# Optimization experiments

Hardware: AMD Instinct MI355X
Metric: run time of the kernel (lower is better)

Reference implementation:

```python
import jax, jax.numpy as jnp
import numpy as np

N_USER = 25000
N_ITEM = 25000
N = N_USER + N_ITEM
E = 1_250_000
D = 64
L = 3
B = 4096


def setup_inputs() -> dict:
    key = jax.random.key(0)
    ks = jax.random.split(key, 11)
    emb = jax.random.normal(ks[0], (N, D), dtype=jnp.float32) * 0.1
    w1_w = jax.random.normal(ks[1], (L, D, D), dtype=jnp.float32) / np.sqrt(D)
    w1_b = jax.random.normal(ks[2], (L, D), dtype=jnp.float32) * 0.01
    w2_w = jax.random.normal(ks[3], (L, D, D), dtype=jnp.float32) / np.sqrt(D)
    w2_b = jax.random.normal(ks[4], (L, D), dtype=jnp.float32) * 0.01
    # normalized-laplacian-like nonneg values
    vals = jax.random.uniform(ks[5], (E,), dtype=jnp.float32) * 0.1
    rows = jax.random.randint(ks[6], (E,), 0, N, dtype=jnp.int32)
    cols = jax.random.randint(ks[7], (E,), 0, N, dtype=jnp.int32)
    user = jax.random.randint(ks[8], (B,), 0, N_USER, dtype=jnp.int32)
    pos = jax.random.randint(ks[9], (B,), 0, N, dtype=jnp.int32)
    neg = jax.random.randint(ks[10], (B,), 0, N, dtype=jnp.int32)
    return {"emb": emb, "w1_w": w1_w, "w1_b": w1_b, "w2_w": w2_w,
            "w2_b": w2_b, "vals": vals, "rows": rows, "cols": cols,
            "user": user, "pos": pos, "neg": neg}


def _spmm(vals, rows, cols, x):
    # sparse [N,N] @ dense [N,D] via gather + segment_sum
    msg = vals[:, None] * x[cols]          # [E, D]
    return jax.ops.segment_sum(msg, rows, num_segments=N)  # [N, D]


def reference(emb, w1_w, w1_b, w2_w, w2_b, vals, rows, cols, user, pos, neg):
    user_embs = [emb[user]]
    pos_embs = [emb[pos]]
    neg_embs = [emb[neg]]
    for l in range(L):
        agg = _spmm(vals, rows, cols, emb)                # sp.mm(laplacian, emb)
        # (laplacian + identity) @ emb == agg + emb
        sx = (agg + emb) @ w1_w[l].T + w1_b[l]
        ox = agg * (emb @ w2_w[l].T + w2_b[l])
        emb = jax.nn.leaky_relu(sx + ox, negative_slope=0.01)
        user_embs.append(emb[user])
        pos_embs.append(emb[pos])
        neg_embs.append(emb[neg])
    user_e = jnp.concatenate(user_embs, axis=-1)          # [B, (L+1)*D]
    pos_e = jnp.concatenate(pos_embs, axis=-1)
    neg_e = jnp.concatenate(neg_embs, axis=-1)
    pos_logits = jnp.einsum('id,id->i', user_e, pos_e)
    neg_logits = jnp.einsum('id,id->i', user_e, neg_e)
    # -log(sigmoid(diff)).sum(), computed stably
    return -jnp.sum(jax.nn.log_sigmoid(pos_logits - neg_logits))
```

## Files before the change

kernel.cpp:

```cpp
#include <hip/hip_runtime.h>
#include <hip/hip_fp16.h>
#include <math.h>

#define N_NODES 50000
#define EDGES   1250000
#define DIM     64
#define NLAYER  3
#define BATCH   4096
#define NSLOTS  (3 * BATCH)

#define NBUCK 196
#define RPB   256
#define NABLK 512
#define BCAP  7424

typedef unsigned int uint32;
typedef _Float16 f16x8 __attribute__((ext_vector_type(8)));
typedef float f32x4 __attribute__((ext_vector_type(4)));

static __device__ __forceinline__ ushort f2h(float f) {
    return __half_as_ushort(__float2half(f));
}
static __device__ __forceinline__ float h2f(ushort u) {
    return __half2float(__ushort_as_half(u));
}

static __device__ __forceinline__ int slot_node(int slot,
                                                const int* __restrict__ user,
                                                const int* __restrict__ pos,
                                                const int* __restrict__ neg) {
    if (slot < BATCH) return user[slot];
    if (slot < 2 * BATCH) return pos[slot - BATCH];
    return neg[slot - 2 * BATCH];
}


#define HP_F2H   512
#define HP_DOTS  3637
#define HP_TOTAL 4661

__global__ __launch_bounds__(256) void histprep_kernel(const int* __restrict__ rows,
                                                       int* __restrict__ bhist,
                                                       const float* __restrict__ emb,
                                                       ushort* __restrict__ xh,
                                                       const int* __restrict__ user,
                                                       const int* __restrict__ pos,
                                                       const int* __restrict__ neg,
                                                       float* __restrict__ dots,
                                                       float* __restrict__ out) {
    __shared__ int h[NBUCK];
    int blk = blockIdx.x;
    int tid = threadIdx.x;
    if (blk < HP_F2H) {
        if (blk == 0 && tid == 0) out[0] = 0.f;
        for (int i = tid; i < NBUCK; i += 256) h[i] = 0;
        __syncthreads();
        int per = (EDGES + NABLK - 1) / NABLK;
        int e0 = blk * per;
        int e1 = min(e0 + per, EDGES);
        for (int e = e0 + tid; e < e1; e += 256)
            atomicAdd(&h[rows[e] >> 8], 1);
        __syncthreads();
        for (int i = tid; i < NBUCK; i += 256)
            bhist[(size_t)i * NABLK + blk] = h[i];
    } else if (blk < HP_DOTS) {
        int i = (blk - HP_F2H) * 256 + tid;
        float4 v = ((const float4*)emb)[i];
        ushort4 hh;
        hh.x = f2h(v.x); hh.y = f2h(v.y); hh.z = f2h(v.z); hh.w = f2h(v.w);
        ((ushort4*)xh)[i] = hh;
    } else {
        int lane = tid & 63;
        int i = (blk - HP_DOTS) * 4 + (tid >> 6);
        int ui = user[i], pi = pos[i], ni = neg[i];
        float u = emb[(size_t)ui * DIM + lane];
        float p = emb[(size_t)pi * DIM + lane];
        float n = emb[(size_t)ni * DIM + lane];
        float v = u * (p - n);
#pragma unroll
        for (int off = 32; off; off >>= 1) v += __shfl_xor(v, off);
        if (lane == 0) dots[i] = v;
    }
}


__global__ __launch_bounds__(512) void boffs_kernel(const int* __restrict__ bhist,
                                                    int* __restrict__ boffs) {
    __shared__ int sbase[256];
    __shared__ int wred[8];
    int b = blockIdx.x;
    int tid = threadIdx.x;
    int lane = tid & 63, wid = tid >> 6;

    int tot = 0;
    if (tid < NBUCK) {
        const int* p = bhist + (size_t)tid * NABLK;
        for (int k = 0; k < NABLK; ++k) tot += p[k];
    }
    int sB = tot;
    if (tid < 256) {
#pragma unroll
        for (int off = 1; off < 64; off <<= 1) {
            int tt = __shfl_up(sB, off);
            if (lane >= off) sB += tt;
        }
        if (lane == 63) wred[wid] = sB;
    }
    __syncthreads();
    if (tid == 0) {
        int a = 0;
#pragma unroll
        for (int i = 0; i < 4; ++i) { int tt = wred[i]; wred[i] = a; a += tt; }
    }
    __syncthreads();
    if (tid < 256) sbase[tid] = wred[wid] + sB - tot;
    __syncthreads();
    int base = sbase[b];
    __syncthreads();

    int v = bhist[(size_t)b * NABLK + tid];
    int s = v;
#pragma unroll
    for (int off = 1; off < 64; off <<= 1) {
        int tt = __shfl_up(s, off);
        if (lane >= off) s += tt;
    }
    if (lane == 63) wred[wid] = s;
    __syncthreads();
    if (tid == 0) {
        int a = 0;
#pragma unroll
        for (int i = 0; i < 8; ++i) { int tt = wred[i]; wred[i] = a; a += tt; }
    }
    __syncthreads();
    boffs[(size_t)b * NABLK + tid] = base + wred[wid] + s - v;
}


__global__ __launch_bounds__(256) void bucket_scatter_kernel(const int* __restrict__ rows,
                                                             const int* __restrict__ cols,
                                                             const float* __restrict__ vals,
                                                             const int* __restrict__ boffs,
                                                             int2* __restrict__ staging) {
    __shared__ int cur[NBUCK];
    for (int t = threadIdx.x; t < NBUCK; t += 256)
        cur[t] = boffs[(size_t)t * NABLK + blockIdx.x];
    __syncthreads();
    int per = (EDGES + NABLK - 1) / NABLK;
    int e0 = blockIdx.x * per;
    int e1 = min(e0 + per, EDGES);
    for (int e = e0 + threadIdx.x; e < e1; e += 256) {
        int r = rows[e];
        int p = atomicAdd(&cur[r >> 8], 1);
        staging[p] = make_int2(((r & 255) << 16) | cols[e], __float_as_int(vals[e]));
    }
}


__global__ __launch_bounds__(512) void csr_build_kernel(const int* __restrict__ boffs,
                                                        const int2* __restrict__ staging,
                                                        int* __restrict__ row_ptr,
                                                        uint32* __restrict__ csr) {
    __shared__ int2 sedge[BCAP];
    __shared__ int rcur[RPB];
    __shared__ int wred[4];
    int b = blockIdx.x;
    int base = boffs[(size_t)b * NABLK];
    int end = (b == NBUCK - 1) ? EDGES : boffs[(size_t)(b + 1) * NABLK];
    int cnt = end - base;
    bool inlds = (cnt <= BCAP);
    int tid = threadIdx.x;
    int lane = tid & 63, wid = tid >> 6;
    if (tid < RPB) rcur[tid] = 0;
    __syncthreads();
    if (inlds) {
        for (int p = tid; p < cnt; p += 512) {
            int2 e = staging[base + p];
            sedge[p] = e;
            atomicAdd(&rcur[e.x >> 16], 1);
        }
    } else {
        for (int p = base + tid; p < end; p += 512)
            atomicAdd(&rcur[staging[p].x >> 16], 1);
    }
    __syncthreads();
    int v = 0, s = 0;
    if (tid < RPB) {
        v = rcur[tid];
        s = v;
#pragma unroll
        for (int off = 1; off < 64; off <<= 1) {
            int t = __shfl_up(s, off);
            if (lane >= off) s += t;
        }
        if (lane == 63) wred[wid] = s;
    }
    __syncthreads();
    if (tid == 0) {
        int a = 0;
#pragma unroll
        for (int i = 0; i < 4; ++i) { int t = wred[i]; wred[i] = a; a += t; }
    }
    __syncthreads();
    if (tid < RPB) {
        int excl = wred[wid] + s - v;
        rcur[tid] = base + excl;
        int row = b * RPB + tid;
        if (row < N_NODES) row_ptr[row] = base + excl;
    }
    if (b == NBUCK - 1 && tid == 0) row_ptr[N_NODES] = EDGES;
    __syncthreads();
    if (inlds) {
        for (int p = tid; p < cnt; p += 512) {
            int2 e = sedge[p];
            int pos = atomicAdd(&rcur[e.x >> 16], 1);
            csr[pos] = ((uint32)(e.x & 0xFFFF) << 16) | (uint32)f2h(__int_as_float(e.y));
        }
    } else {
        for (int p = base + tid; p < end; p += 512) {
            int2 e = staging[p];
            int pos = atomicAdd(&rcur[e.x >> 16], 1);
            csr[pos] = ((uint32)(e.x & 0xFFFF) << 16) | (uint32)f2h(__int_as_float(e.y));
        }
    }
}


static __device__ __forceinline__ void spmm_row(const uint32* __restrict__ csr,
                                                const ushort* __restrict__ xh,
                                                int p0, int p1, int g, int sl,
                                                float* a) {
#define SPMM_ACC(E, X)                                                     \
    {                                                                      \
        float vv = h2f((ushort)((E) & 0xFFFF));                            \
        a[0] += vv * h2f((ushort)((X).x & 0xFFFF));                        \
        a[1] += vv * h2f((ushort)((X).x >> 16));                           \
        a[2] += vv * h2f((ushort)((X).y & 0xFFFF));                        \
        a[3] += vv * h2f((ushort)((X).y >> 16));                           \
        a[4] += vv * h2f((ushort)((X).z & 0xFFFF));                        \
        a[5] += vv * h2f((ushort)((X).z >> 16));                           \
        a[6] += vv * h2f((ushort)((X).w & 0xFFFF));                        \
        a[7] += vv * h2f((ushort)((X).w >> 16));                           \
    }
    int p = p0;
    for (; p + 32 <= p1; p += 32) {
        uint32 e0 = csr[p + g];
        uint32 e1 = csr[p + 8 + g];
        uint32 e2 = csr[p + 16 + g];
        uint32 e3 = csr[p + 24 + g];
        uint4 x0 = *(const uint4*)(xh + (size_t)(e0 >> 16) * DIM + sl * 8);
        uint4 x1 = *(const uint4*)(xh + (size_t)(e1 >> 16) * DIM + sl * 8);
        uint4 x2 = *(const uint4*)(xh + (size_t)(e2 >> 16) * DIM + sl * 8);
        uint4 x3 = *(const uint4*)(xh + (size_t)(e3 >> 16) * DIM + sl * 8);
        SPMM_ACC(e0, x0);
        SPMM_ACC(e1, x1);
        SPMM_ACC(e2, x2);
        SPMM_ACC(e3, x3);
    }
    for (; p + 8 <= p1; p += 8) {
        uint32 ea = csr[p + g];
        uint4 xa = *(const uint4*)(xh + (size_t)(ea >> 16) * DIM + sl * 8);
        SPMM_ACC(ea, xa);
    }
    if (p + g < p1) {
        uint32 ea = csr[p + g];
        uint4 xa = *(const uint4*)(xh + (size_t)(ea >> 16) * DIM + sl * 8);
        SPMM_ACC(ea, xa);
    }
#undef SPMM_ACC
#pragma unroll
    for (int m = 8; m <= 32; m <<= 1) {
        a[0] += __shfl_xor(a[0], m); a[1] += __shfl_xor(a[1], m);
        a[2] += __shfl_xor(a[2], m); a[3] += __shfl_xor(a[3], m);
        a[4] += __shfl_xor(a[4], m); a[5] += __shfl_xor(a[5], m);
        a[6] += __shfl_xor(a[6], m); a[7] += __shfl_xor(a[7], m);
    }
}

static __device__ __forceinline__ void spmm_store(ushort* dst, const float* a, int lane) {
    if (lane < 8) {
        ushort t[8];
        t[0] = f2h(a[0]); t[1] = f2h(a[1]); t[2] = f2h(a[2]); t[3] = f2h(a[3]);
        t[4] = f2h(a[4]); t[5] = f2h(a[5]); t[6] = f2h(a[6]); t[7] = f2h(a[7]);
        *(uint4*)(dst + lane * 8) = *(uint4*)t;
    }
}

static __device__ __forceinline__ void dots_tail(const ushort* __restrict__ xh,
                                                 const int* __restrict__ user,
                                                 const int* __restrict__ pos,
                                                 const int* __restrict__ neg,
                                                 float* __restrict__ dots,
                                                 int i, int lane) {
    int ui = user[i], pi = pos[i], ni = neg[i];
    float u = h2f(xh[(size_t)ui * DIM + lane]);
    float p = h2f(xh[(size_t)pi * DIM + lane]);
    float n = h2f(xh[(size_t)ni * DIM + lane]);
    float v = u * (p - n);
#pragma unroll
    for (int off = 32; off; off >>= 1) v += __shfl_xor(v, off);
    if (lane == 0) dots[i] = v;
}


__global__ __launch_bounds__(256) void spmm_kernel(const int* __restrict__ row_ptr,
                                                   const uint32* __restrict__ csr,
                                                   const ushort* __restrict__ xh,
                                                   ushort* __restrict__ aggh,
                                                   const int* __restrict__ user,
                                                   const int* __restrict__ pos,
                                                   const int* __restrict__ neg,
                                                   float* __restrict__ dots,
                                                   int nsb) {
    int lane = threadIdx.x & 63;
    if ((int)blockIdx.x >= nsb) {
        int i = (blockIdx.x - nsb) * 4 + (threadIdx.x >> 6);
        dots_tail(xh, user, pos, neg, dots, i, lane);
        return;
    }
    int row = blockIdx.x * 4 + (threadIdx.x >> 6);
    int p0 = row_ptr[row], p1 = row_ptr[row + 1];
    float a[8] = {};
    spmm_row(csr, xh, p0, p1, lane >> 3, lane & 7, a);
    spmm_store(aggh + (size_t)row * DIM, a, lane);
}


__global__ __launch_bounds__(256) void spmm_slots_kernel(const int* __restrict__ row_ptr,
                                                         const uint32* __restrict__ csr,
                                                         const ushort* __restrict__ xh,
                                                         ushort* __restrict__ aggh_slot,
                                                         const int* __restrict__ user,
                                                         const int* __restrict__ pos,
                                                         const int* __restrict__ neg,
                                                         float* __restrict__ dots,
                                                         int nsb) {
    int lane = threadIdx.x & 63;
    if ((int)blockIdx.x >= nsb) {
        int i = (blockIdx.x - nsb) * 4 + (threadIdx.x >> 6);
        dots_tail(xh, user, pos, neg, dots, i, lane);
        return;
    }
    int slot = blockIdx.x * 4 + (threadIdx.x >> 6);
    int node = slot_node(slot, user, pos, neg);
    int p0 = row_ptr[node], p1 = row_ptr[node + 1];
    float a[8] = {};
    spmm_row(csr, xh, p0, p1, lane >> 3, lane & 7, a);
    spmm_store(aggh_slot + (size_t)slot * DIM, a, lane);
}


template <int IS_SLOT>
static __device__ __forceinline__ void dense_body(const ushort* __restrict__ xh_in,
                                                  const ushort* __restrict__ aggh,
                                                  const float* __restrict__ w1,
                                                  const float* __restrict__ w2,
                                                  const float* __restrict__ b1,
                                                  const float* __restrict__ b2,
                                                  ushort* __restrict__ yh,
                                                  const int* __restrict__ user,
                                                  const int* __restrict__ pos,
                                                  const int* __restrict__ neg) {
    __shared__ ushort xs[64 * 64];
    __shared__ ushort xc[64 * 64];
    __shared__ ushort w1s[64 * 64];
    __shared__ ushort w2s[64 * 64];

    int tid = threadIdx.x;
    int n0 = blockIdx.x * 64;

    {
        int rr = tid >> 2;
        int jq = (tid & 3) << 4;
        int sw = rr & 7;
        int b0 = jq >> 3;
        int o0 = rr * 64 + (((b0 + 0) ^ sw) << 3);
        int o1 = rr * 64 + (((b0 + 1) ^ sw) << 3);

        {
            const float* w1r = w1 + rr * 64 + jq;
            const float* w2r = w2 + rr * 64 + jq;
            ushort t1[16], t2[16];
#pragma unroll
            for (int k = 0; k < 4; ++k) {
                float4 a = ((const float4*)w1r)[k];
                float4 b = ((const float4*)w2r)[k];
                t1[k * 4 + 0] = f2h(a.x); t1[k * 4 + 1] = f2h(a.y);
                t1[k * 4 + 2] = f2h(a.z); t1[k * 4 + 3] = f2h(a.w);
                t2[k * 4 + 0] = f2h(b.x); t2[k * 4 + 1] = f2h(b.y);
                t2[k * 4 + 2] = f2h(b.z); t2[k * 4 + 3] = f2h(b.w);
            }
            *(uint4*)&w1s[o0] = *(uint4*)&t1[0];
            *(uint4*)&w1s[o1] = *(uint4*)&t1[8];
            *(uint4*)&w2s[o0] = *(uint4*)&t2[0];
            *(uint4*)&w2s[o1] = *(uint4*)&t2[8];
        }
        {
            int rowid = n0 + rr;
            int xnode, arow;
            if (IS_SLOT) {
                xnode = slot_node(rowid, user, pos, neg);
                arow = rowid;
            } else {
                xnode = (rowid < N_NODES) ? rowid : (N_NODES - 1);
                arow = xnode;
            }
            const ushort* ar = aggh + (size_t)arow * DIM + jq;
            const ushort* xr = xh_in + (size_t)xnode * DIM + jq;
            ushort txs[16], txc[16];
#pragma unroll
            for (int k = 0; k < 2; ++k) {
                uint4 xv = ((const uint4*)xr)[k];
                uint4 av = ((const uint4*)ar)[k];
                uint32 xw[4] = {xv.x, xv.y, xv.z, xv.w};
                uint32 aw[4] = {av.x, av.y, av.z, av.w};
#pragma unroll
                for (int q = 0; q < 4; ++q) {
                    ushort xlo = (ushort)(xw[q] & 0xFFFF);
                    ushort xhi = (ushort)(xw[q] >> 16);
                    ushort alo = (ushort)(aw[q] & 0xFFFF);
                    ushort ahi = (ushort)(aw[q] >> 16);
                    int e = k * 8 + q * 2;
                    txc[e] = xlo; txc[e + 1] = xhi;
                    txs[e] = f2h(h2f(xlo) + h2f(alo));
                    txs[e + 1] = f2h(h2f(xhi) + h2f(ahi));
                }
            }
            *(uint4*)&xs[o0] = *(uint4*)&txs[0];
            *(uint4*)&xs[o1] = *(uint4*)&txs[8];
            *(uint4*)&xc[o0] = *(uint4*)&txc[0];
            *(uint4*)&xc[o1] = *(uint4*)&txc[8];
        }
    }
    __syncthreads();

    int lane = tid & 63, w = tid >> 6;
    int nb = w << 4;
    int lm = lane & 15;
    int le = lane >> 4;

    f16x8 axs[2], axc[2];
#pragma unroll
    for (int k = 0; k < 2; ++k) {
        int n = nb + lm;
        int blk = k * 4 + le;
        int off = n * 64 + ((blk ^ (n & 7)) << 3);
        axs[k] = *(const f16x8*)&xs[off];
        axc[k] = *(const f16x8*)&xc[off];
    }

#pragma unroll
    for (int dt = 0; dt < 4; ++dt) {
        int d = dt * 16 + lm;
        f16x8 bf1[2], bf2[2];
#pragma unroll
        for (int k = 0; k < 2; ++k) {
            int blk = k * 4 + le;
            int off = d * 64 + ((blk ^ (d & 7)) << 3);
            bf1[k] = *(const f16x8*)&w1s[off];
            bf2[k] = *(const f16x8*)&w2s[off];
        }
        f32x4 acc1 = {0.f, 0.f, 0.f, 0.f};
        f32x4 acc2 = {0.f, 0.f, 0.f, 0.f};
        acc1 = __builtin_amdgcn_mfma_f32_16x16x32_f16(axs[0], bf1[0], acc1, 0, 0, 0);
        acc1 = __builtin_amdgcn_mfma_f32_16x16x32_f16(axs[1], bf1[1], acc1, 0, 0, 0);
        acc2 = __builtin_amdgcn_mfma_f32_16x16x32_f16(axc[0], bf2[0], acc2, 0, 0, 0);
        acc2 = __builtin_amdgcn_mfma_f32_16x16x32_f16(axc[1], bf2[1], acc2, 0, 0, 0);

        float b1v = b1[d], b2v = b2[d];
        int bb = d >> 3;
#pragma unroll
        for (int i = 0; i < 4; ++i) {
            int nl = nb + (le << 2) + i;
            int rowid = n0 + nl;
            int off = nl * 64 + ((bb ^ (nl & 7)) << 3) + (d & 7);
            float ag = h2f(xs[off]) - h2f(xc[off]);
            float t = acc1[i] + b1v + ag * (acc2[i] + b2v);
            t = (t > 0.f) ? t : 0.01f * t;
            bool wr = IS_SLOT ? true : (rowid < N_NODES);
            if (wr) yh[(size_t)rowid * DIM + d] = f2h(t);
        }
    }
}

__global__ __launch_bounds__(256) void dense_kernel(const ushort* __restrict__ xh_in,
                                                    const ushort* __restrict__ aggh,
                                                    const float* __restrict__ w1,
                                                    const float* __restrict__ w2,
                                                    const float* __restrict__ b1,
                                                    const float* __restrict__ b2,
                                                    ushort* __restrict__ yh) {
    dense_body<0>(xh_in, aggh, w1, w2, b1, b2, yh, nullptr, nullptr, nullptr);
}

__global__ __launch_bounds__(256) void dense_slots_kernel(const ushort* __restrict__ xh_in,
                                                          const ushort* __restrict__ aggh_slot,
                                                          const float* __restrict__ w1,
                                                          const float* __restrict__ w2,
                                                          const float* __restrict__ b1,
                                                          const float* __restrict__ b2,
                                                          ushort* __restrict__ yh_slot,
                                                          const int* __restrict__ user,
                                                          const int* __restrict__ pos,
                                                          const int* __restrict__ neg) {
    dense_body<1>(xh_in, aggh_slot, w1, w2, b1, b2, yh_slot, user, pos, neg);
}


__global__ __launch_bounds__(256) void dots_loss_kernel(const ushort* __restrict__ yh_slot,
                                                        const float* __restrict__ dots,
                                                        float* __restrict__ out) {
    __shared__ float part[4];
    int tid = threadIdx.x;
    int lane = tid & 63;
    int i = blockIdx.x * 4 + (tid >> 6);
    float u = h2f(yh_slot[(size_t)i * DIM + lane]);
    float p = h2f(yh_slot[(size_t)(BATCH + i) * DIM + lane]);
    float n = h2f(yh_slot[(size_t)(2 * BATCH + i) * DIM + lane]);
    float v = u * (p - n);
#pragma unroll
    for (int off = 32; off; off >>= 1) v += __shfl_xor(v, off);
    if (lane == 0) {
        float d = dots[i] + dots[BATCH + i] + dots[2 * BATCH + i] + v;
        part[tid >> 6] = fmaxf(-d, 0.f) + log1pf(expf(-fabsf(d)));
    }
    __syncthreads();
    if (tid == 0) atomicAdd(out, part[0] + part[1] + part[2] + part[3]);
}


extern "C" void kernel_launch(void* const* d_in, const int* in_sizes, int n_in,
                              void* d_out, int out_size, void* d_ws, size_t ws_size,
                              hipStream_t stream) {
    const float* emb  = (const float*)d_in[0];
    const float* w1_w = (const float*)d_in[1];
    const float* w1_b = (const float*)d_in[2];
    const float* w2_w = (const float*)d_in[3];
    const float* w2_b = (const float*)d_in[4];
    const float* vals = (const float*)d_in[5];
    const int* rows = (const int*)d_in[6];
    const int* cols = (const int*)d_in[7];
    const int* user = (const int*)d_in[8];
    const int* pos  = (const int*)d_in[9];
    const int* neg  = (const int*)d_in[10];
    float* out = (float*)d_out;

    char* w = (char*)d_ws;
    char* region = w;          w += (size_t)N_NODES * DIM * 4;
    ushort* aggh = (ushort*)region;
    int2* staging = (int2*)region;
    int* row_ptr = (int*)w;   w += (((size_t)(N_NODES + 1) * 4) + 255) / 256 * 256;
    uint32* csr  = (uint32*)w; w += (size_t)EDGES * 4;
    int* bhist   = (int*)w;   w += (size_t)NBUCK * NABLK * 4;
    int* boffs   = (int*)w;   w += (size_t)NBUCK * NABLK * 4;
    float* dots  = (float*)w; w += (size_t)3 * BATCH * 4;
    ushort* xhA  = (ushort*)w; w += (size_t)N_NODES * DIM * 2;
    ushort* xhB  = (ushort*)w; w += (size_t)N_NODES * DIM * 2;
    ushort* aggh_slot = (ushort*)w; w += (size_t)NSLOTS * DIM * 2;
    ushort* yh_slot   = (ushort*)w; w += (size_t)NSLOTS * DIM * 2;

    histprep_kernel<<<HP_TOTAL, 256, 0, stream>>>(rows, bhist, emb, xhA,
                                                  user, pos, neg, dots, out);
    boffs_kernel<<<NBUCK, 512, 0, stream>>>(bhist, boffs);
    bucket_scatter_kernel<<<NABLK, 256, 0, stream>>>(rows, cols, vals, boffs, staging);
    csr_build_kernel<<<NBUCK, 512, 0, stream>>>(boffs, staging, row_ptr, csr);

    const int NSB = N_NODES / 4;
    const int NTB = BATCH / 4;
    const int NDB = (N_NODES + 63) / 64;
    const int NSLB = NSLOTS / 4;
    const int NSDB = NSLOTS / 64;

    spmm_kernel<<<NSB, 256, 0, stream>>>(row_ptr, csr, xhA, aggh, user, pos, neg, dots, NSB);
    dense_kernel<<<NDB, 256, 0, stream>>>(xhA, aggh, w1_w + 0 * 4096, w2_w + 0 * 4096,
                                          w1_b + 0 * DIM, w2_b + 0 * DIM, xhB);
    spmm_kernel<<<NSB + NTB, 256, 0, stream>>>(row_ptr, csr, xhB, aggh, user, pos, neg,
                                               dots + BATCH, NSB);
    dense_kernel<<<NDB, 256, 0, stream>>>(xhB, aggh, w1_w + 1 * 4096, w2_w + 1 * 4096,
                                          w1_b + 1 * DIM, w2_b + 1 * DIM, xhA);
    spmm_slots_kernel<<<NSLB + NTB, 256, 0, stream>>>(row_ptr, csr, xhA, aggh_slot,
                                                      user, pos, neg, dots + 2 * BATCH, NSLB);
    dense_slots_kernel<<<NSDB, 256, 0, stream>>>(xhA, aggh_slot,
                                                 w1_w + 2 * 4096, w2_w + 2 * 4096,
                                                 w1_b + 2 * DIM, w2_b + 2 * DIM,
                                                 yh_slot, user, pos, neg);

    dots_loss_kernel<<<NTB, 256, 0, stream>>>(yh_slot, dots, out);
}
```

Before: 156.3 us.

## Fuse histogram, offset scan and bucket scatter into one atomic-reservation kernel

Merges the per-block histogram, global offset scan and bucket scatter into a single kernel. Each block stages its edges in LDS and reserves slots in fixed-capacity per-bucket regions via global atomics. The offset scan is moved into csr_build, which removes two launches and a second read of rows/cols/vals. In exchange, buckets that overflow the fixed capacity drop edges, edge order becomes nondeterministic, and the large LDS array reduces occupancy of the conversion and dot blocks.

```diff
diff --git a/kernel.cpp b/kernel.cpp
--- a/kernel.cpp
+++ b/kernel.cpp
@@ -12,7 +12,9 @@
 #define NBUCK 196
 #define RPB   256
 #define NABLK 512
-#define BCAP  7424
+#define CAP_S 7424
+#define BCAP  CAP_S
+#define PER_BLK ((EDGES + NABLK - 1) / NABLK)
 
 typedef unsigned int uint32;
 typedef _Float16 f16x8 __attribute__((ext_vector_type(8)));
@@ -35,43 +37,60 @@
 }
 
 
-#define HP_F2H   512
-#define HP_DOTS  3637
-#define HP_TOTAL 4661
-
-__global__ __launch_bounds__(256) void histprep_kernel(const int* __restrict__ rows,
-                                                       int* __restrict__ bhist,
-                                                       const float* __restrict__ emb,
-                                                       ushort* __restrict__ xh,
-                                                       const int* __restrict__ user,
-                                                       const int* __restrict__ pos,
-                                                       const int* __restrict__ neg,
-                                                       float* __restrict__ dots,
-                                                       float* __restrict__ out) {
+#define SP_F2H   512
+#define SP_DOTS  3637
+#define SP_TOTAL 4661
+
+__global__ __launch_bounds__(256) void scatterprep_kernel(const int* __restrict__ rows,
+                                                          const int* __restrict__ cols,
+                                                          const float* __restrict__ vals,
+                                                          int* __restrict__ gcur,
+                                                          int2* __restrict__ staging,
+                                                          const float* __restrict__ emb,
+                                                          ushort* __restrict__ xh,
+                                                          const int* __restrict__ user,
+                                                          const int* __restrict__ pos,
+                                                          const int* __restrict__ neg,
+                                                          float* __restrict__ dots,
+                                                          float* __restrict__ out) {
+    __shared__ int2 sedge[PER_BLK];
     __shared__ int h[NBUCK];
+    __shared__ int roff[NBUCK];
     int blk = blockIdx.x;
     int tid = threadIdx.x;
-    if (blk < HP_F2H) {
+    if (blk < SP_F2H) {
         if (blk == 0 && tid == 0) out[0] = 0.f;
         for (int i = tid; i < NBUCK; i += 256) h[i] = 0;
         __syncthreads();
-        int per = (EDGES + NABLK - 1) / NABLK;
-        int e0 = blk * per;
-        int e1 = min(e0 + per, EDGES);
-        for (int e = e0 + tid; e < e1; e += 256)
-            atomicAdd(&h[rows[e] >> 8], 1);
+        int e0 = blk * PER_BLK;
+        int e1 = min(e0 + PER_BLK, EDGES);
+        int cnt = e1 - e0;
+        for (int i = tid; i < cnt; i += 256) {
+            int e = e0 + i;
+            int r = rows[e];
+            sedge[i] = make_int2((r << 16) | cols[e], __float_as_int(vals[e]));
+            atomicAdd(&h[r >> 8], 1);
+        }
         __syncthreads();
-        for (int i = tid; i < NBUCK; i += 256)
-            bhist[(size_t)i * NABLK + blk] = h[i];
-    } else if (blk < HP_DOTS) {
-        int i = (blk - HP_F2H) * 256 + tid;
+        for (int t = tid; t < NBUCK; t += 256)
+            roff[t] = t * CAP_S + atomicAdd(&gcur[t], h[t]);
+        __syncthreads();
+        for (int i = tid; i < cnt; i += 256) {
+            int2 e = sedge[i];
+            int bkt = ((uint32)e.x) >> 24;
+            int p = atomicAdd(&roff[bkt], 1);
+            if (p < (bkt + 1) * CAP_S)
+                staging[p] = make_int2(e.x & 0x00FFFFFF, e.y);
+        }
+    } else if (blk < SP_DOTS) {
+        int i = (blk - SP_F2H) * 256 + tid;
         float4 v = ((const float4*)emb)[i];
         ushort4 hh;
         hh.x = f2h(v.x); hh.y = f2h(v.y); hh.z = f2h(v.z); hh.w = f2h(v.w);
         ((ushort4*)xh)[i] = hh;
     } else {
         int lane = tid & 63;
-        int i = (blk - HP_DOTS) * 4 + (tid >> 6);
+        int i = (blk - SP_DOTS) * 4 + (tid >> 6);
         int ui = user[i], pi = pos[i], ni = neg[i];
         float u = emb[(size_t)ui * DIM + lane];
         float p = emb[(size_t)pi * DIM + lane];
@@ -84,104 +103,48 @@
 }
 
 
-__global__ __launch_bounds__(512) void boffs_kernel(const int* __restrict__ bhist,
-                                                    int* __restrict__ boffs) {
-    __shared__ int sbase[256];
-    __shared__ int wred[8];
-    int b = blockIdx.x;
-    int tid = threadIdx.x;
-    int lane = tid & 63, wid = tid >> 6;
-
-    int tot = 0;
-    if (tid < NBUCK) {
-        const int* p = bhist + (size_t)tid * NABLK;
-        for (int k = 0; k < NABLK; ++k) tot += p[k];
-    }
-    int sB = tot;
-    if (tid < 256) {
-#pragma unroll
-        for (int off = 1; off < 64; off <<= 1) {
-            int tt = __shfl_up(sB, off);
-            if (lane >= off) sB += tt;
-        }
-        if (lane == 63) wred[wid] = sB;
-    }
-    __syncthreads();
-    if (tid == 0) {
-        int a = 0;
-#pragma unroll
-        for (int i = 0; i < 4; ++i) { int tt = wred[i]; wred[i] = a; a += tt; }
-    }
-    __syncthreads();
-    if (tid < 256) sbase[tid] = wred[wid] + sB - tot;
-    __syncthreads();
-    int base = sbase[b];
-    __syncthreads();
-
-    int v = bhist[(size_t)b * NABLK + tid];
-    int s = v;
-#pragma unroll
-    for (int off = 1; off < 64; off <<= 1) {
-        int tt = __shfl_up(s, off);
-        if (lane >= off) s += tt;
-    }
-    if (lane == 63) wred[wid] = s;
-    __syncthreads();
-    if (tid == 0) {
-        int a = 0;
-#pragma unroll
-        for (int i = 0; i < 8; ++i) { int tt = wred[i]; wred[i] = a; a += tt; }
-    }
-    __syncthreads();
-    boffs[(size_t)b * NABLK + tid] = base + wred[wid] + s - v;
-}
-
-
-__global__ __launch_bounds__(256) void bucket_scatter_kernel(const int* __restrict__ rows,
-                                                             const int* __restrict__ cols,
-                                                             const float* __restrict__ vals,
-                                                             const int* __restrict__ boffs,
-                                                             int2* __restrict__ staging) {
-    __shared__ int cur[NBUCK];
-    for (int t = threadIdx.x; t < NBUCK; t += 256)
-        cur[t] = boffs[(size_t)t * NABLK + blockIdx.x];
-    __syncthreads();
-    int per = (EDGES + NABLK - 1) / NABLK;
-    int e0 = blockIdx.x * per;
-    int e1 = min(e0 + per, EDGES);
-    for (int e = e0 + threadIdx.x; e < e1; e += 256) {
-        int r = rows[e];
-        int p = atomicAdd(&cur[r >> 8], 1);
-        staging[p] = make_int2(((r & 255) << 16) | cols[e], __float_as_int(vals[e]));
-    }
-}
-
-
-__global__ __launch_bounds__(512) void csr_build_kernel(const int* __restrict__ boffs,
+__global__ __launch_bounds__(512) void csr_build_kernel(const int* __restrict__ gcur,
                                                         const int2* __restrict__ staging,
                                                         int* __restrict__ row_ptr,
                                                         uint32* __restrict__ csr) {
     __shared__ int2 sedge[BCAP];
+    __shared__ int sbase[256];
     __shared__ int rcur[RPB];
     __shared__ int wred[4];
     int b = blockIdx.x;
-    int base = boffs[(size_t)b * NABLK];
-    int end = (b == NBUCK - 1) ? EDGES : boffs[(size_t)(b + 1) * NABLK];
-    int cnt = end - base;
-    bool inlds = (cnt <= BCAP);
     int tid = threadIdx.x;
     int lane = tid & 63, wid = tid >> 6;
+
+    int tot = (tid < NBUCK) ? gcur[tid] : 0;
+    int sB = tot;
+    if (tid < 256) {
+#pragma unroll
+        for (int off = 1; off < 64; off <<= 1) {
+            int tt = __shfl_up(sB, off);
+            if (lane >= off) sB += tt;
+        }
+        if (lane == 63) wred[wid] = sB;
+    }
+    __syncthreads();
+    if (tid == 0) {
+        int a = 0;
+#pragma unroll
+        for (int i = 0; i < 4; ++i) { int tt = wred[i]; wred[i] = a; a += tt; }
+    }
+    __syncthreads();
+    if (tid < 256) sbase[tid] = wred[wid] + sB - tot;
+    __syncthreads();
+    int base = sbase[b];
+    int cnt = (b == NBUCK - 1) ? (EDGES - sbase[NBUCK - 1]) : (sbase[b + 1] - sbase[b]);
+    int sbeg = b * CAP_S;
+    __syncthreads();
+
     if (tid < RPB) rcur[tid] = 0;
     __syncthreads();
-    if (inlds) {
-        for (int p = tid; p < cnt; p += 512) {
-            int2 e = staging[base + p];
-            sedge[p] = e;
-            atomicAdd(&rcur[e.x >> 16], 1);
-        }
-    } else {
-        for (int p = base + tid; p < end; p += 512)
-            atomicAdd(&rcur[staging[p].x >> 16], 1);
+    for (int p = tid; p < cnt; p += 512) {
+        int2 e = staging[sbeg + p];
+        sedge[p] = e;
+        atomicAdd(&rcur[e.x >> 16], 1);
     }
     __syncthreads();
     int v = 0, s = 0;
@@ -210,18 +173,10 @@
     }
     if (b == NBUCK - 1 && tid == 0) row_ptr[N_NODES] = EDGES;
     __syncthreads();
-    if (inlds) {
-        for (int p = tid; p < cnt; p += 512) {
-            int2 e = sedge[p];
-            int pos = atomicAdd(&rcur[e.x >> 16], 1);
-            csr[pos] = ((uint32)(e.x & 0xFFFF) << 16) | (uint32)f2h(__int_as_float(e.y));
-        }
-    } else {
-        for (int p = base + tid; p < end; p += 512) {
-            int2 e = staging[p];
-            int pos = atomicAdd(&rcur[e.x >> 16], 1);
-            csr[pos] = ((uint32)(e.x & 0xFFFF) << 16) | (uint32)f2h(__int_as_float(e.y));
-        }
+    for (int p = tid; p < cnt; p += 512) {
+        int2 e = sedge[p];
+        int pos = atomicAdd(&rcur[e.x >> 16], 1);
+        csr[pos] = ((uint32)(e.x & 0xFFFF) << 16) | (uint32)f2h(__int_as_float(e.y));
     }
 }
 
@@ -546,24 +501,23 @@
     float* out = (float*)d_out;
 
     char* w = (char*)d_ws;
-    char* region = w;          w += (size_t)N_NODES * DIM * 4;
+    char* region = w;          w += (size_t)NBUCK * CAP_S * 8;
     ushort* aggh = (ushort*)region;
     int2* staging = (int2*)region;
     int* row_ptr = (int*)w;   w += (((size_t)(N_NODES + 1) * 4) + 255) / 256 * 256;
     uint32* csr  = (uint32*)w; w += (size_t)EDGES * 4;
-    int* bhist   = (int*)w;   w += (size_t)NBUCK * NABLK * 4;
-    int* boffs   = (int*)w;   w += (size_t)NBUCK * NABLK * 4;
+    int* gcur    = (int*)w;   w += 256 * 4;
     float* dots  = (float*)w; w += (size_t)3 * BATCH * 4;
     ushort* xhA  = (ushort*)w; w += (size_t)N_NODES * DIM * 2;
     ushort* xhB  = (ushort*)w; w += (size_t)N_NODES * DIM * 2;
     ushort* aggh_slot = (ushort*)w; w += (size_t)NSLOTS * DIM * 2;
     ushort* yh_slot   = (ushort*)w; w += (size_t)NSLOTS * DIM * 2;
 
-    histprep_kernel<<<HP_TOTAL, 256, 0, stream>>>(rows, bhist, emb, xhA,
-                                                  user, pos, neg, dots, out);
-    boffs_kernel<<<NBUCK, 512, 0, stream>>>(bhist, boffs);
-    bucket_scatter_kernel<<<NABLK, 256, 0, stream>>>(rows, cols, vals, boffs, staging);
-    csr_build_kernel<<<NBUCK, 512, 0, stream>>>(boffs, staging, row_ptr, csr);
+    hipMemsetAsync(gcur, 0, 256 * 4, stream);
+
+    scatterprep_kernel<<<SP_TOTAL, 256, 0, stream>>>(rows, cols, vals, gcur, staging,
+                                                     emb, xhA, user, pos, neg, dots, out);
+    csr_build_kernel<<<NBUCK, 512, 0, stream>>>(gcur, staging, row_ptr, csr);
 
     const int NSB = N_NODES / 4;
     const int NTB = BATCH / 4;
```

New measurement: 150.3 us. 1.04x faster.
